# Kernel tuning notes

Measured on AMD Instinct MI355X. Metric: run time of the kernel, lower is better.

The kernel has to match this reference:

```python
import jax, jax.numpy as jnp
import numpy as np

B, S, H, NH = 2, 2048, 1024, 16
DH = H // NH           # attention_head_size = 64
EPS = 1e-12            # layer_norm_eps
THR = 0.1              # noise_threshold
SCALE = 1.0 / np.sqrt(DH).astype(np.float32)


def _ortho(k, n):
    q, _ = jnp.linalg.qr(jax.random.normal(k, (n, n)))
    return q.astype(jnp.float32)


def setup_inputs() -> dict:
    key = jax.random.key(0)
    ks = jax.random.split(key, 16)
    s = 0.02
    return {
        "hidden_states": jax.random.normal(ks[0], (B, S, H), dtype=jnp.float32),
        "Wq": jax.random.normal(ks[1], (DH, 2 * DH), dtype=jnp.float32) * s,
        "bq": jnp.zeros((2 * DH,), jnp.float32),
        "Wk": jax.random.normal(ks[2], (DH, 2 * DH), dtype=jnp.float32) * s,
        "bk": jnp.zeros((2 * DH,), jnp.float32),
        "Wv": jax.random.normal(ks[3], (DH, 2 * DH), dtype=jnp.float32) * s,
        "bv": jnp.zeros((2 * DH,), jnp.float32),
        "Uq_r": _ortho(ks[4], DH), "Uq_i": jnp.zeros((DH, DH), jnp.float32),
        "Uk_r": _ortho(ks[5], DH), "Uk_i": jnp.zeros((DH, DH), jnp.float32),
        "Uv_r": _ortho(ks[6], DH), "Uv_i": jnp.zeros((DH, DH), jnp.float32),
        "Wo": jax.random.normal(ks[7], (H, H), dtype=jnp.float32) * s,
        "bo": jnp.zeros((H,), jnp.float32),
        "gamma": jnp.ones((H,), jnp.float32),
        "beta": jnp.zeros((H,), jnp.float32),
    }


def _prep(x, W, b):
    # QuantumStatePreparation: linear dh->2dh, chunk into (real, imag),
    # per-element normalize to unit magnitude.
    c = x @ W + b
    r, i = jnp.split(c, 2, axis=-1)
    n = jnp.sqrt(r * r + i * i + 1e-12)
    return r / n, i / n


def _gate(ri, Ur, Ui):
    # QuantumGate: complex matmul (r + j*i) @ (Ur + j*Ui) in real arithmetic.
    r, i = ri
    return r @ Ur - i @ Ui, r @ Ui + i @ Ur


def reference(hidden_states, Wq, bq, Wk, bk, Wv, bv,
              Uq_r, Uq_i, Uk_r, Uk_i, Uv_r, Uv_i,
              Wo, bo, gamma, beta):
    b, s, _ = hidden_states.shape
    x = hidden_states.reshape(b, s, NH, DH).transpose(0, 2, 1, 3)  # [B,NH,S,DH]

    qr, qi = _gate(_prep(x, Wq, bq), Uq_r, Uq_i)
    kr, ki = _gate(_prep(x, Wk, bk), Uk_r, Uk_i)
    vr, vi = _gate(_prep(x, Wv, bv), Uv_r, Uv_i)

    # complex scores q @ k^T (no conjugate, as in the torch code)
    sr = jnp.einsum("bhqd,bhkd->bhqk", qr, kr) - jnp.einsum("bhqd,bhkd->bhqk", qi, ki)
    si = jnp.einsum("bhqd,bhkd->bhqk", qr, ki) + jnp.einsum("bhqd,bhkd->bhqk", qi, kr)
    mag = jnp.sqrt(sr * sr + si * si) * SCALE       # |scores / sqrt(dh)|
    scores = jnp.where(mag < THR, 0.0, mag)         # threshold-masked magnitude
    probs = jax.nn.softmax(scores, axis=-1)         # dropout is identity (eval)

    v_mag = jnp.sqrt(vr * vr + vi * vi)             # torch.abs of complex value
    ctx = jnp.einsum("bhqk,bhkd->bhqd", probs, v_mag)
    ctx = ctx.transpose(0, 2, 1, 3).reshape(b, s, H)

    out = ctx @ Wo + bo
    res = out + hidden_states
    mu = jnp.mean(res, axis=-1, keepdims=True)
    var = jnp.mean((res - mu) ** 2, axis=-1, keepdims=True)
    normed = (res - mu) / jnp.sqrt(var + EPS) * gamma + beta
    return normed, probs
```

## Files before the change

kernel.cpp:

```cpp
#include <hip/hip_runtime.h>
#include <math.h>


#define B_  2
#define S_  2048
#define H_  1024
#define NH_ 16
#define DH_ 64
#define NELEM    4194304
#define NORMEDSZ 4194304

typedef __attribute__((ext_vector_type(8))) short bf16x8;
typedef __attribute__((ext_vector_type(4))) float f32x4;

__device__ __forceinline__ ushort f2bf(float x) {
  uint u = __float_as_uint(x);
  u += 0x7fffu + ((u >> 16) & 1u);
  return (ushort)(u >> 16);
}
__device__ __forceinline__ float bf2f(ushort h) {
  return __uint_as_float(((uint)h) << 16);
}

__global__ __launch_bounds__(256, 4) void k_prep_gate(
    const float* __restrict__ hidden,
    const float* __restrict__ Wq, const float* __restrict__ bq,
    const float* __restrict__ Wk, const float* __restrict__ bk,
    const float* __restrict__ Wv, const float* __restrict__ bv,
    const float* __restrict__ Uqr, const float* __restrict__ Uqi,
    const float* __restrict__ Ukr, const float* __restrict__ Uki,
    const float* __restrict__ Uvr, const float* __restrict__ Uvi,
    ushort* __restrict__ qrP, ushort* __restrict__ qiP,
    ushort* __restrict__ krP, ushort* __restrict__ kiP,
    float* __restrict__ vm)
{
  const int bid = blockIdx.x;
  const int st  = bid & 63;
  const int h   = (bid >> 6) & 15;
  const int b   = bid >> 10;
  const int s0  = st * 32;
  const int tid = threadIdx.x;
  const int j   = tid & 63;
  const int tg  = tid >> 6;

  __shared__ float xs[32][64];
  __shared__ float rb[32][64];
  __shared__ float ib[32][64];

  for (int i = 0; i < 8; ++i) {
    int f = tid + i * 256;
    int t = f >> 6, d = f & 63;
    xs[t][d] = hidden[((b * S_ + s0 + t) * H_) + h * 64 + d];
  }
  __syncthreads();

  const float* Ws[3]  = {Wq, Wk, Wv};
  const float* bs[3]  = {bq, bk, bv};
  const float* Urs[3] = {Uqr, Ukr, Uvr};
  const float* Uis[3] = {Uqi, Uki, Uvi};
  const int bh   = b * NH_ + h;
  const int head = bh * S_ * DH_;

  for (int m = 0; m < 3; ++m) {
    const float* W  = Ws[m];
    const float* bb = bs[m];
    const float* Ur = Urs[m];
    const float* Ui = Uis[m];

    float cr[8], ci[8];
    const float bj0 = bb[j], bj1 = bb[64 + j];
#pragma unroll
    for (int p = 0; p < 8; ++p) { cr[p] = bj0; ci[p] = bj1; }
    for (int d = 0; d < 64; ++d) {
      float wr = W[d * 128 + j];
      float wi = W[d * 128 + 64 + j];
#pragma unroll
      for (int p = 0; p < 8; ++p) {
        float x = xs[tg * 8 + p][d];
        cr[p] = fmaf(x, wr, cr[p]);
        ci[p] = fmaf(x, wi, ci[p]);
      }
    }
#pragma unroll
    for (int p = 0; p < 8; ++p) {
      float inv = rsqrtf(cr[p] * cr[p] + ci[p] * ci[p] + 1e-12f);
      rb[tg * 8 + p][j] = cr[p] * inv;
      ib[tg * 8 + p][j] = ci[p] * inv;
    }
    __syncthreads();

    float gr[8] = {0.f,0.f,0.f,0.f,0.f,0.f,0.f,0.f};
    float gi[8] = {0.f,0.f,0.f,0.f,0.f,0.f,0.f,0.f};
    for (int d = 0; d < 64; ++d) {
      float ur = Ur[d * 64 + j];
      float ui = Ui[d * 64 + j];
#pragma unroll
      for (int p = 0; p < 8; ++p) {
        float rv = rb[tg * 8 + p][d];
        float iv = ib[tg * 8 + p][d];
        gr[p] = fmaf(rv, ur, fmaf(-iv, ui, gr[p]));
        gi[p] = fmaf(rv, ui, fmaf( iv, ur, gi[p]));
      }
    }
    if (m == 2) {
#pragma unroll
      for (int p = 0; p < 8; ++p) {
        int t = tg * 8 + p;
        vm[head + (s0 + t) * DH_ + j] = sqrtf(gr[p] * gr[p] + gi[p] * gi[p]);
      }
    } else {
      ushort* R = (m == 0) ? qrP : krP;
      ushort* I = (m == 0) ? qiP : kiP;
#pragma unroll
      for (int p = 0; p < 8; ++p) {
        int t = tg * 8 + p;
        size_t pb = (((size_t)bh) * S_ + (s0 + t)) * 128 + j;
        ushort hr = f2bf(gr[p]);
        R[pb]      = hr;
        R[pb + 64] = f2bf(gr[p] - bf2f(hr));
        ushort hi2 = f2bf(gi[p]);
        I[pb]      = hi2;
        I[pb + 64] = f2bf(gi[p] - bf2f(hi2));
      }
    }
    __syncthreads();
  }
}

#define MFMA16 __builtin_amdgcn_mfma_f32_16x16x32_bf16

__global__ __launch_bounds__(256, 2) void k_scores_mfma(
    const ushort* __restrict__ qrP, const ushort* __restrict__ qiP,
    const ushort* __restrict__ krP, const ushort* __restrict__ kiP,
    float* __restrict__ praw, float* __restrict__ lsum)
{
  const int bid0 = blockIdx.x;
  const int bid  = (bid0 & 7) * 128 + (bid0 >> 3);
  const int qt = bid & 31;
  const int bh = bid >> 5;
  const int q0 = qt * 64;
  const int tid  = threadIdx.x;
  const int lane = tid & 63;
  const int w    = tid >> 6;
  const int wq   = w & 1;
  const int wk   = w >> 1;
  const int l15  = lane & 15;
  const int lg   = lane >> 4;

  __shared__ __align__(16) ushort skr[64 * 128];
  __shared__ __align__(16) ushort ski[64 * 128];
  __shared__ float lsh[64];
  if (tid < 64) lsh[tid] = 0.f;

  bf16x8 aqr[2][4], aqi[2][4];
#pragma unroll
  for (int rt = 0; rt < 2; ++rt) {
    const size_t ro = ((size_t)bh * S_ + q0 + wq * 32 + rt * 16 + l15) * 128 + lg * 8;
#pragma unroll
    for (int ks = 0; ks < 4; ++ks) {
      aqr[rt][ks] = *(const bf16x8*)(qrP + ro + ks * 32);
      aqi[rt][ks] = *(const bf16x8*)(qiP + ro + ks * 32);
    }
  }

  float esum[2][4] = {{0.f,0.f,0.f,0.f},{0.f,0.f,0.f,0.f}};

  const int swz = (l15 & 7) << 4;
  const int kbB = (wk * 32 + l15) * 256;

  for (int kt = 0; kt < 32; ++kt) {
    __syncthreads();
    {
      const uint4* gr4 = (const uint4*)(krP + ((size_t)bh * S_ + kt * 64) * 128);
      const uint4* gi4 = (const uint4*)(kiP + ((size_t)bh * S_ + kt * 64) * 128);
#pragma unroll
      for (int i = 0; i < 4; ++i) {
        int c   = tid + i * 256;
        int key = c >> 4;
        int dq  = c & 15;
        int dst = (key * 256 + dq * 16) ^ ((key & 7) << 4);
        *(uint4*)((char*)skr + dst) = gr4[c];
        *(uint4*)((char*)ski + dst) = gi4[c];
      }
    }
    __syncthreads();

    f32x4 aRR[2][2], aII[2][2], aRI[2][2], aIR[2][2];
#pragma unroll
    for (int rt = 0; rt < 2; ++rt)
#pragma unroll
      for (int ct = 0; ct < 2; ++ct) {
        aRR[rt][ct] = (f32x4){0.f,0.f,0.f,0.f};
        aII[rt][ct] = (f32x4){0.f,0.f,0.f,0.f};
        aRI[rt][ct] = (f32x4){0.f,0.f,0.f,0.f};
        aIR[rt][ct] = (f32x4){0.f,0.f,0.f,0.f};
      }

#pragma unroll
    for (int ks = 0; ks < 4; ++ks) {
#pragma unroll
      for (int ct = 0; ct < 2; ++ct) {
        const int o = kbB + ct * 4096 + ((ks * 64 + lg * 16) ^ swz);
        bf16x8 br = *(const bf16x8*)((const char*)skr + o);
        bf16x8 bi = *(const bf16x8*)((const char*)ski + o);
#pragma unroll
        for (int rt = 0; rt < 2; ++rt) {
          aRR[rt][ct] = MFMA16(aqr[rt][ks], br, aRR[rt][ct], 0, 0, 0);
          aIR[rt][ct] = MFMA16(aqi[rt][ks], br, aIR[rt][ct], 0, 0, 0);
          aRI[rt][ct] = MFMA16(aqr[rt][ks], bi, aRI[rt][ct], 0, 0, 0);
          aII[rt][ct] = MFMA16(aqi[rt][ks], bi, aII[rt][ct], 0, 0, 0);
        }
      }
    }

    const size_t rowb = ((size_t)bh * S_ + q0 + wq * 32) * S_
                      + (size_t)kt * 64 + wk * 32 + l15;
#pragma unroll
    for (int rt = 0; rt < 2; ++rt)
#pragma unroll
      for (int r = 0; r < 4; ++r) {
        const int rloc = rt * 16 + lg * 4 + r;
        float sr0 = aRR[rt][0][r] - aII[rt][0][r];
        float si0 = aRI[rt][0][r] + aIR[rt][0][r];
        float m0 = sqrtf(sr0 * sr0 + si0 * si0) * 0.125f;
        m0 = (m0 < 0.1f) ? 0.f : m0;
        float e0 = __expf(m0);
        float sr1 = aRR[rt][1][r] - aII[rt][1][r];
        float si1 = aRI[rt][1][r] + aIR[rt][1][r];
        float m1 = sqrtf(sr1 * sr1 + si1 * si1) * 0.125f;
        m1 = (m1 < 0.1f) ? 0.f : m1;
        float e1 = __expf(m1);
        praw[rowb + (size_t)rloc * S_]      = e0;
        praw[rowb + (size_t)rloc * S_ + 16] = e1;
        esum[rt][r] += e0 + e1;
      }
  }

#pragma unroll
  for (int rt = 0; rt < 2; ++rt)
#pragma unroll
    for (int r = 0; r < 4; ++r) {
      float v = esum[rt][r];
      v += __shfl_xor(v, 1, 64);
      v += __shfl_xor(v, 2, 64);
      v += __shfl_xor(v, 4, 64);
      v += __shfl_xor(v, 8, 64);
      if (l15 == 0) atomicAdd(&lsh[wq * 32 + rt * 16 + lg * 4 + r], v);
    }
  __syncthreads();
  if (tid < 64) lsum[(size_t)bh * S_ + q0 + tid] = lsh[tid];
}

#define SPST 65

__global__ __launch_bounds__(256, 4) void k_pv(
    const float* __restrict__ vm, const float* __restrict__ lsum,
    float* __restrict__ probs, float* __restrict__ ctx)
{
  const int bid = blockIdx.x;
  const int qt  = bid & 31;
  const int bh  = bid >> 5;
  const int q0  = qt * 64;
  const int b   = bh >> 4, h = bh & 15;
  const int tid = threadIdx.x;
  const int rg  = tid >> 4;
  const int dg  = tid & 15;
  const int r0  = rg * 4;
  const int d0  = dg * 4;
  const int head = bh * (S_ * DH_);

  __shared__ float sp[64 * SPST];
  __shared__ __align__(16) float svm[64 * 64];
  __shared__ float rinv[64];
  if (tid < 64) rinv[tid] = 1.f / lsum[bh * S_ + q0 + tid];

  float acc[4][4] = {{0.f,0.f,0.f,0.f},{0.f,0.f,0.f,0.f},
                     {0.f,0.f,0.f,0.f},{0.f,0.f,0.f,0.f}};

  for (int kt = 0; kt < 32; ++kt) {
    __syncthreads();
    for (int i = 0; i < 16; ++i) {
      int f = tid + i * 256;
      int r = f >> 6, c = f & 63;
      size_t off = ((size_t)bh * S_ + q0 + r) * S_ + kt * 64 + c;
      float p = probs[off] * rinv[r];
      probs[off] = p;
      sp[r * SPST + c] = p;
    }
    for (int i = 0; i < 4; ++i) {
      int g = tid + i * 256;
      int c = g >> 4, dq = g & 15;
      *(float4*)(svm + c * 64 + dq * 4) =
          *(const float4*)(vm + head + (kt * 64 + c) * 64 + dq * 4);
    }
    __syncthreads();

    for (int ck = 0; ck < 64; ++ck) {
      const float4 v4 = *(const float4*)(svm + ck * 64 + d0);
#pragma unroll
      for (int jr = 0; jr < 4; ++jr) {
        float p = sp[(r0 + jr) * SPST + ck];
        acc[jr][0] = fmaf(p, v4.x, acc[jr][0]);
        acc[jr][1] = fmaf(p, v4.y, acc[jr][1]);
        acc[jr][2] = fmaf(p, v4.z, acc[jr][2]);
        acc[jr][3] = fmaf(p, v4.w, acc[jr][3]);
      }
    }
  }
#pragma unroll
  for (int jr = 0; jr < 4; ++jr) {
    float4 o;
    o.x = acc[jr][0]; o.y = acc[jr][1]; o.z = acc[jr][2]; o.w = acc[jr][3];
    *(float4*)(ctx + (size_t)(b * S_ + q0 + r0 + jr) * H_ + h * 64 + d0) = o;
  }
}

#define AST 36
#define BST 68

__global__ __launch_bounds__(256, 4) void k_out_gemm(
    const float* __restrict__ ctx, const float* __restrict__ Wo,
    const float* __restrict__ bo, const float* __restrict__ hidden,
    float* __restrict__ res)
{
  const int bid = blockIdx.x;
  const int nt  = bid & 15;
  const int mt  = bid >> 4;
  const int m0  = mt * 64, n0 = nt * 64;
  const int tid = threadIdx.x;
  const int mg  = tid >> 4, ng = tid & 15;

  __shared__ __align__(16) float sa[64 * AST];
  __shared__ __align__(16) float sb[32 * BST];

  float acc[4][4] = {{0.f,0.f,0.f,0.f},{0.f,0.f,0.f,0.f},
                     {0.f,0.f,0.f,0.f},{0.f,0.f,0.f,0.f}};

  for (int kt = 0; kt < 32; ++kt) {
    __syncthreads();
    for (int i = 0; i < 2; ++i) {
      int g = tid + i * 256;
      int r = g >> 3, dq = g & 7;
      *(float4*)(sa + r * AST + dq * 4) =
          *(const float4*)(ctx + (size_t)(m0 + r) * H_ + kt * 32 + dq * 4);
    }
    for (int i = 0; i < 2; ++i) {
      int g = tid + i * 256;
      int r = g >> 4, dq = g & 15;
      *(float4*)(sb + r * BST + dq * 4) =
          *(const float4*)(Wo + (size_t)(kt * 32 + r) * H_ + n0 + dq * 4);
    }
    __syncthreads();

    for (int kk = 0; kk < 32; ++kk) {
      const float4 b4 = *(const float4*)(sb + kk * BST + ng * 4);
      const float a0 = sa[(mg * 4 + 0) * AST + kk];
      const float a1 = sa[(mg * 4 + 1) * AST + kk];
      const float a2 = sa[(mg * 4 + 2) * AST + kk];
      const float a3 = sa[(mg * 4 + 3) * AST + kk];
      acc[0][0] = fmaf(a0, b4.x, acc[0][0]); acc[0][1] = fmaf(a0, b4.y, acc[0][1]);
      acc[0][2] = fmaf(a0, b4.z, acc[0][2]); acc[0][3] = fmaf(a0, b4.w, acc[0][3]);
      acc[1][0] = fmaf(a1, b4.x, acc[1][0]); acc[1][1] = fmaf(a1, b4.y, acc[1][1]);
      acc[1][2] = fmaf(a1, b4.z, acc[1][2]); acc[1][3] = fmaf(a1, b4.w, acc[1][3]);
      acc[2][0] = fmaf(a2, b4.x, acc[2][0]); acc[2][1] = fmaf(a2, b4.y, acc[2][1]);
      acc[2][2] = fmaf(a2, b4.z, acc[2][2]); acc[2][3] = fmaf(a2, b4.w, acc[2][3]);
      acc[3][0] = fmaf(a3, b4.x, acc[3][0]); acc[3][1] = fmaf(a3, b4.y, acc[3][1]);
      acc[3][2] = fmaf(a3, b4.z, acc[3][2]); acc[3][3] = fmaf(a3, b4.w, acc[3][3]);
    }
  }

  const float4 bo4 = *(const float4*)(bo + n0 + ng * 4);
#pragma unroll
  for (int jm = 0; jm < 4; ++jm) {
    int m = m0 + mg * 4 + jm;
    const float4 hv = *(const float4*)(hidden + (size_t)m * H_ + n0 + ng * 4);
    float4 o;
    o.x = acc[jm][0] + bo4.x + hv.x;
    o.y = acc[jm][1] + bo4.y + hv.y;
    o.z = acc[jm][2] + bo4.z + hv.z;
    o.w = acc[jm][3] + bo4.w + hv.w;
    *(float4*)(res + (size_t)m * H_ + n0 + ng * 4) = o;
  }
}

__global__ __launch_bounds__(256, 4) void k_layernorm(
    const float* __restrict__ gamma, const float* __restrict__ beta,
    float* __restrict__ out)
{
  const int t   = blockIdx.x;
  const int tid = threadIdx.x;
  float4 x = *(const float4*)(out + (size_t)t * H_ + tid * 4);
  float s = x.x + x.y + x.z + x.w;
  float q = x.x * x.x + x.y * x.y + x.z * x.z + x.w * x.w;
  for (int off = 32; off > 0; off >>= 1) {
    s += __shfl_down(s, off, 64);
    q += __shfl_down(q, off, 64);
  }
  __shared__ float red[8];
  int wid = tid >> 6;
  if ((tid & 63) == 0) { red[wid] = s; red[4 + wid] = q; }
  __syncthreads();
  s = red[0] + red[1] + red[2] + red[3];
  q = red[4] + red[5] + red[6] + red[7];
  const float mu  = s * (1.f / 1024.f);
  const float var = fmaxf(q * (1.f / 1024.f) - mu * mu, 0.f);
  const float rstd = rsqrtf(var + 1e-12f);
  const float4 g4 = *(const float4*)(gamma + tid * 4);
  const float4 b4 = *(const float4*)(beta + tid * 4);
  float4 o;
  o.x = (x.x - mu) * rstd * g4.x + b4.x;
  o.y = (x.y - mu) * rstd * g4.y + b4.y;
  o.z = (x.z - mu) * rstd * g4.z + b4.z;
  o.w = (x.w - mu) * rstd * g4.w + b4.w;
  *(float4*)(out + (size_t)t * H_ + tid * 4) = o;
}

extern "C" void kernel_launch(void* const* d_in, const int* in_sizes, int n_in,
                              void* d_out, int out_size, void* d_ws, size_t ws_size,
                              hipStream_t stream) {
  (void)in_sizes; (void)n_in; (void)out_size; (void)ws_size;

  const float* hidden = (const float*)d_in[0];
  const float* Wq  = (const float*)d_in[1];  const float* bq = (const float*)d_in[2];
  const float* Wk  = (const float*)d_in[3];  const float* bk = (const float*)d_in[4];
  const float* Wv  = (const float*)d_in[5];  const float* bv = (const float*)d_in[6];
  const float* Uqr = (const float*)d_in[7];  const float* Uqi = (const float*)d_in[8];
  const float* Ukr = (const float*)d_in[9];  const float* Uki = (const float*)d_in[10];
  const float* Uvr = (const float*)d_in[11]; const float* Uvi = (const float*)d_in[12];
  const float* Wo  = (const float*)d_in[13]; const float* bo = (const float*)d_in[14];
  const float* gamma = (const float*)d_in[15];
  const float* beta  = (const float*)d_in[16];

  float* outp  = (float*)d_out;
  float* probs = outp + NORMEDSZ;

  float* ws = (float*)d_ws;
  ushort* qrP = (ushort*)(ws);
  ushort* qiP = (ushort*)(ws + (size_t)NELEM);
  ushort* krP = (ushort*)(ws + 2 * (size_t)NELEM);
  ushort* kiP = (ushort*)(ws + 3 * (size_t)NELEM);
  float*  vm  = ws + 4 * (size_t)NELEM;
  float*  ls  = ws + 5 * (size_t)NELEM;
  float*  ctx = ws;

  k_prep_gate<<<2048, 256, 0, stream>>>(hidden, Wq, bq, Wk, bk, Wv, bv,
                                        Uqr, Uqi, Ukr, Uki, Uvr, Uvi,
                                        qrP, qiP, krP, kiP, vm);
  k_scores_mfma<<<1024, 256, 0, stream>>>(qrP, qiP, krP, kiP, probs, ls);
  k_pv<<<1024, 256, 0, stream>>>(vm, ls, probs, ctx);
  k_out_gemm<<<1024, 256, 0, stream>>>(ctx, Wo, bo, hidden, outp);
  k_layernorm<<<4096, 256, 0, stream>>>(gamma, beta, outp);
}
```

Baseline: 1.577 ms.

## Move P·V onto bf16 split-precision MFMA with transposed V magnitude layout

The PV kernel's scalar FP32 FMA inner loop is replaced by bf16x3 split-precision MFMA (hi·hi + hi·lo + lo·hi). Probabilities are converted to hi/lo bf16 in XOR-swizzled shared memory while being normalized and written back with float4 accesses. The prep kernel now stores |V| transposed (d-major) as hi/lo bf16 pairs. Block order is remapped for locality. The cost is extra conversion work and slightly lower precision than FP32, in exchange for matrix-core throughput.

```diff
diff --git a/kernel.cpp b/kernel.cpp
--- a/kernel.cpp
+++ b/kernel.cpp
@@ -11,6 +11,7 @@
 #define NORMEDSZ 4194304
 
 typedef __attribute__((ext_vector_type(8))) short bf16x8;
+typedef __attribute__((ext_vector_type(8))) ushort u16x8;
 typedef __attribute__((ext_vector_type(4))) float f32x4;
 
 __device__ __forceinline__ ushort f2bf(float x) {
@@ -32,7 +33,7 @@
     const float* __restrict__ Uvr, const float* __restrict__ Uvi,
     ushort* __restrict__ qrP, ushort* __restrict__ qiP,
     ushort* __restrict__ krP, ushort* __restrict__ kiP,
-    float* __restrict__ vm)
+    ushort* __restrict__ vmH, ushort* __restrict__ vmL)
 {
   const int bid = blockIdx.x;
   const int st  = bid & 63;
@@ -59,7 +60,6 @@
   const float* Urs[3] = {Uqr, Ukr, Uvr};
   const float* Uis[3] = {Uqi, Uki, Uvi};
   const int bh   = b * NH_ + h;
-  const int head = bh * S_ * DH_;
 
   for (int m = 0; m < 3; ++m) {
     const float* W  = Ws[m];
@@ -103,11 +103,24 @@
       }
     }
     if (m == 2) {
-#pragma unroll
-      for (int p = 0; p < 8; ++p) {
-        int t = tg * 8 + p;
-        vm[head + (s0 + t) * DH_ + j] = sqrtf(gr[p] * gr[p] + gi[p] * gi[p]);
-      }
+      __syncthreads();
+#pragma unroll
+      for (int p = 0; p < 8; ++p)
+        rb[tg * 8 + p][j] = sqrtf(gr[p] * gr[p] + gi[p] * gi[p]);
+      __syncthreads();
+      const int d  = tid >> 2;
+      const int c4 = tid & 3;
+      u16x8 hv8, lv8;
+#pragma unroll
+      for (int tt = 0; tt < 8; ++tt) {
+        float v = rb[c4 * 8 + tt][d];
+        ushort hv = f2bf(v);
+        hv8[tt] = hv;
+        lv8[tt] = f2bf(v - bf2f(hv));
+      }
+      const size_t o = ((size_t)(bh * 64 + d)) * S_ + s0 + c4 * 8;
+      *(u16x8*)(vmH + o) = hv8;
+      *(u16x8*)(vmL + o) = lv8;
     } else {
       ushort* R = (m == 0) ? qrP : krP;
       ushort* I = (m == 0) ? qiP : kiP;
@@ -251,68 +264,110 @@
   if (tid < 64) lsum[(size_t)bh * S_ + q0 + tid] = lsh[tid];
 }
 
-#define SPST 65
-
-__global__ __launch_bounds__(256, 4) void k_pv(
-    const float* __restrict__ vm, const float* __restrict__ lsum,
+__global__ __launch_bounds__(256, 4) void k_pv_mfma(
+    const ushort* __restrict__ vmH, const ushort* __restrict__ vmL,
+    const float* __restrict__ lsum,
     float* __restrict__ probs, float* __restrict__ ctx)
 {
-  const int bid = blockIdx.x;
-  const int qt  = bid & 31;
-  const int bh  = bid >> 5;
-  const int q0  = qt * 64;
-  const int b   = bh >> 4, h = bh & 15;
-  const int tid = threadIdx.x;
-  const int rg  = tid >> 4;
-  const int dg  = tid & 15;
-  const int r0  = rg * 4;
-  const int d0  = dg * 4;
-  const int head = bh * (S_ * DH_);
-
-  __shared__ float sp[64 * SPST];
-  __shared__ __align__(16) float svm[64 * 64];
+  const int bid0 = blockIdx.x;
+  const int bid  = (bid0 & 7) * 128 + (bid0 >> 3);
+  const int qt = bid & 31;
+  const int bh = bid >> 5;
+  const int q0 = qt * 64;
+  const int b  = bh >> 4, h = bh & 15;
+  const int tid  = threadIdx.x;
+  const int lane = tid & 63;
+  const int w    = tid >> 6;
+  const int wq   = w & 1;
+  const int wd   = w >> 1;
+  const int l15  = lane & 15;
+  const int lg   = lane >> 4;
+
+  __shared__ __align__(16) ushort spH[64 * 64];
+  __shared__ __align__(16) ushort spL[64 * 64];
+  __shared__ __align__(16) ushort svH[64 * 64];
+  __shared__ __align__(16) ushort svL[64 * 64];
   __shared__ float rinv[64];
-  if (tid < 64) rinv[tid] = 1.f / lsum[bh * S_ + q0 + tid];
-
-  float acc[4][4] = {{0.f,0.f,0.f,0.f},{0.f,0.f,0.f,0.f},
-                     {0.f,0.f,0.f,0.f},{0.f,0.f,0.f,0.f}};
+  if (tid < 64) rinv[tid] = 1.f / lsum[(size_t)bh * S_ + q0 + tid];
+
+  f32x4 acc[2][2];
+#pragma unroll
+  for (int rt = 0; rt < 2; ++rt)
+#pragma unroll
+    for (int ct = 0; ct < 2; ++ct) acc[rt][ct] = (f32x4){0.f,0.f,0.f,0.f};
+
+  const int swz = (l15 & 7) << 4;
 
   for (int kt = 0; kt < 32; ++kt) {
     __syncthreads();
-    for (int i = 0; i < 16; ++i) {
+#pragma unroll
+    for (int i = 0; i < 4; ++i) {
       int f = tid + i * 256;
-      int r = f >> 6, c = f & 63;
-      size_t off = ((size_t)bh * S_ + q0 + r) * S_ + kt * 64 + c;
-      float p = probs[off] * rinv[r];
-      probs[off] = p;
-      sp[r * SPST + c] = p;
-    }
+      int r = f >> 4, cq = f & 15;
+      size_t off = ((size_t)bh * S_ + q0 + r) * S_ + kt * 64 + cq * 4;
+      float4 e4 = *(const float4*)(probs + off);
+      float ri = rinv[r];
+      float4 p4;
+      p4.x = e4.x * ri; p4.y = e4.y * ri; p4.z = e4.z * ri; p4.w = e4.w * ri;
+      *(float4*)(probs + off) = p4;
+      ushort h0 = f2bf(p4.x), h1 = f2bf(p4.y), h2 = f2bf(p4.z), h3 = f2bf(p4.w);
+      uint2 hp, lp;
+      hp.x = (uint)h0 | ((uint)h1 << 16);
+      hp.y = (uint)h2 | ((uint)h3 << 16);
+      lp.x = (uint)f2bf(p4.x - bf2f(h0)) | ((uint)f2bf(p4.y - bf2f(h1)) << 16);
+      lp.y = (uint)f2bf(p4.z - bf2f(h2)) | ((uint)f2bf(p4.w - bf2f(h3)) << 16);
+      int dst = (r * 128 + cq * 8) ^ ((r & 7) << 4);
+      *(uint2*)((char*)spH + dst) = hp;
+      *(uint2*)((char*)spL + dst) = lp;
+    }
+#pragma unroll
     for (int i = 0; i < 4; ++i) {
-      int g = tid + i * 256;
-      int c = g >> 4, dq = g & 15;
-      *(float4*)(svm + c * 64 + dq * 4) =
-          *(const float4*)(vm + head + (kt * 64 + c) * 64 + dq * 4);
-    }
-    __syncthreads();
-
-    for (int ck = 0; ck < 64; ++ck) {
-      const float4 v4 = *(const float4*)(svm + ck * 64 + d0);
-#pragma unroll
-      for (int jr = 0; jr < 4; ++jr) {
-        float p = sp[(r0 + jr) * SPST + ck];
-        acc[jr][0] = fmaf(p, v4.x, acc[jr][0]);
-        acc[jr][1] = fmaf(p, v4.y, acc[jr][1]);
-        acc[jr][2] = fmaf(p, v4.z, acc[jr][2]);
-        acc[jr][3] = fmaf(p, v4.w, acc[jr][3]);
-      }
-    }
-  }
-#pragma unroll
-  for (int jr = 0; jr < 4; ++jr) {
-    float4 o;
-    o.x = acc[jr][0]; o.y = acc[jr][1]; o.z = acc[jr][2]; o.w = acc[jr][3];
-    *(float4*)(ctx + (size_t)(b * S_ + q0 + r0 + jr) * H_ + h * 64 + d0) = o;
-  }
+      int c = tid + (i & 1) * 256;
+      int d = c >> 3, ch = c & 7;
+      size_t src = ((size_t)(bh * 64 + d)) * S_ + kt * 64 + ch * 8;
+      int dst = (d * 128 + ch * 16) ^ ((d & 7) << 4);
+      if (i < 2) *(uint4*)((char*)svH + dst) = *(const uint4*)(vmH + src);
+      else       *(uint4*)((char*)svL + dst) = *(const uint4*)(vmL + src);
+    }
+    __syncthreads();
+
+#pragma unroll
+    for (int ks = 0; ks < 2; ++ks) {
+      const int co = (ks * 64 + lg * 16) ^ swz;
+      bf16x8 aH[2], aL[2], bH[2], bL[2];
+#pragma unroll
+      for (int rt = 0; rt < 2; ++rt) {
+        const int qrow = wq * 32 + rt * 16 + l15;
+        aH[rt] = *(const bf16x8*)((const char*)spH + qrow * 128 + co);
+        aL[rt] = *(const bf16x8*)((const char*)spL + qrow * 128 + co);
+      }
+#pragma unroll
+      for (int ct = 0; ct < 2; ++ct) {
+        const int drow = wd * 32 + ct * 16 + l15;
+        bH[ct] = *(const bf16x8*)((const char*)svH + drow * 128 + co);
+        bL[ct] = *(const bf16x8*)((const char*)svL + drow * 128 + co);
+      }
+#pragma unroll
+      for (int rt = 0; rt < 2; ++rt)
+#pragma unroll
+        for (int ct = 0; ct < 2; ++ct) {
+          acc[rt][ct] = MFMA16(aH[rt], bH[ct], acc[rt][ct], 0, 0, 0);
+          acc[rt][ct] = MFMA16(aH[rt], bL[ct], acc[rt][ct], 0, 0, 0);
+          acc[rt][ct] = MFMA16(aL[rt], bH[ct], acc[rt][ct], 0, 0, 0);
+        }
+    }
+  }
+
+#pragma unroll
+  for (int rt = 0; rt < 2; ++rt)
+#pragma unroll
+    for (int ct = 0; ct < 2; ++ct)
+#pragma unroll
+      for (int j = 0; j < 4; ++j) {
+        int q = q0 + wq * 32 + rt * 16 + lg * 4 + j;
+        int dcol = h * 64 + wd * 32 + ct * 16 + l15;
+        ctx[(size_t)(b * S_ + q) * H_ + dcol] = acc[rt][ct][j];
+      }
 }
 
 #define AST 36
@@ -439,15 +494,16 @@
   ushort* qiP = (ushort*)(ws + (size_t)NELEM);
   ushort* krP = (ushort*)(ws + 2 * (size_t)NELEM);
   ushort* kiP = (ushort*)(ws + 3 * (size_t)NELEM);
-  float*  vm  = ws + 4 * (size_t)NELEM;
+  ushort* vmH = (ushort*)(ws + 4 * (size_t)NELEM);
+  ushort* vmL = vmH + (size_t)NELEM;
   float*  ls  = ws + 5 * (size_t)NELEM;
   float*  ctx = ws;
 
   k_prep_gate<<<2048, 256, 0, stream>>>(hidden, Wq, bq, Wk, bk, Wv, bv,
                                         Uqr, Uqi, Ukr, Uki, Uvr, Uvi,
-                                        qrP, qiP, krP, kiP, vm);
+                                        qrP, qiP, krP, kiP, vmH, vmL);
   k_scores_mfma<<<1024, 256, 0, stream>>>(qrP, qiP, krP, kiP, probs, ls);
-  k_pv<<<1024, 256, 0, stream>>>(vm, ls, probs, ctx);
+  k_pv_mfma<<<1024, 256, 0, stream>>>(vmH, vmL, ls, probs, ctx);
   k_out_gemm<<<1024, 256, 0, stream>>>(ctx, Wo, bo, hidden, outp);
   k_layernorm<<<4096, 256, 0, stream>>>(gamma, beta, outp);
 }
```

New measurement: 1.266 ms. 1.25x faster.
